# Optimization experiments

Hardware: AMD Instinct MI355X
Metric: run time of the kernel (lower is better)

Reference implementation:

```python
import jax, jax.numpy as jnp
import numpy as np

N_NODES = 20000
N_EDGES = 320000
D_IN = 256
N_CLASS = 10

def _glorot(key, shape):
    fan_in, fan_out = shape[0], shape[1]
    lim = np.sqrt(6.0 / (fan_in + fan_out)).astype(np.float32)
    return jax.random.uniform(key, shape, jnp.float32, -lim, lim)

def setup_inputs() -> dict:
    key = jax.random.key(0)
    ks = jax.random.split(key, 12)
    x = jax.random.normal(ks[0], (N_NODES, D_IN), jnp.float32)
    edge_index = jax.random.randint(ks[1], (2, N_EDGES), 0, N_NODES, jnp.int64)
    return {
        "x": x,
        "edge_index": edge_index,
        # GraphConv 1: num_feature -> 128 (lin_rel on aggregated neighbors, lin_root on self)
        "W1_rel": _glorot(ks[2], (D_IN, 128)),
        "W1_root": _glorot(ks[3], (D_IN, 128)),
        "b1": jnp.zeros((128,), jnp.float32),
        # GraphConv 2: 128 -> 64
        "W2_rel": _glorot(ks[4], (128, 64)),
        "W2_root": _glorot(ks[5], (128, 64)),
        "b2": jnp.zeros((64,), jnp.float32),
        # MLP head
        "lin1_w": _glorot(ks[6], (64, 128)),
        "lin1_b": jnp.zeros((128,), jnp.float32),
        "lin2_w": _glorot(ks[7], (128, 64)),
        "lin2_b": jnp.zeros((64,), jnp.float32),
        "lin3_w": _glorot(ks[8], (64, N_CLASS)),
        "lin3_b": jnp.zeros((N_CLASS,), jnp.float32),
    }

def _graph_conv(x, src, dst, W_rel, W_root, b):
    # PyG GraphConv (aggr='add'): out_i = W_rel @ sum_{j in N(i)} x_j + W_root @ x_i + b
    agg = jax.ops.segment_sum(x[src], dst, num_segments=x.shape[0])  # [N, d_in]
    return agg @ W_rel + x @ W_root + b

def reference(x, edge_index, W1_rel, W1_root, b1, W2_rel, W2_root, b2,
              lin1_w, lin1_b, lin2_w, lin2_b, lin3_w, lin3_b):
    src, dst = edge_index[0], edge_index[1]  # flow: source_to_target
    h = _graph_conv(x, src, dst, W1_rel, W1_root, b1)
    h = jax.nn.relu(h)  # dropout is identity in eval mode
    h = _graph_conv(h, src, dst, W2_rel, W2_root, b2)
    h = jax.nn.relu(h @ lin1_w + lin1_b)
    h = jax.nn.relu(h @ lin2_w + lin2_b)
    return jax.nn.log_softmax(h @ lin3_w + lin3_b, axis=-1)
```

## Files before the change

kernel.cpp:

```cpp
#include <hip/hip_runtime.h>


#define NNODES 20000
#define NEDGES 320000
#define CAP 64

typedef __attribute__((ext_vector_type(8))) short bf16x8;
typedef __attribute__((ext_vector_type(4))) float f32x4;

__device__ inline short f2bf(float f) {
    unsigned u = __builtin_bit_cast(unsigned, f);
    u += 0x7FFFu + ((u >> 16) & 1u);
    return (short)(u >> 16);
}
__device__ inline float bf2f(short h) {
    unsigned u = ((unsigned)(unsigned short)h) << 16;
    return __builtin_bit_cast(float, u);
}

__device__ inline size_t swz_off(int n, int k, int ktiles) {
    return (size_t)((n >> 4) * ktiles + (k >> 5)) * 512 +
           ((((k >> 3) & 3) * 16 + (n & 15)) << 3) + (k & 7);
}

__global__ void prep_kernel(const float* __restrict__ W1r, const float* __restrict__ W1o,
                            const float* __restrict__ W2r, const float* __restrict__ W2o,
                            const float* __restrict__ L1,  const float* __restrict__ L2,
                            short* __restrict__ WT,
                            const float* __restrict__ x, short* __restrict__ XBs,
                            const int* __restrict__ src, const int* __restrict__ dst,
                            int* __restrict__ cnt, int* __restrict__ nbr) {
    const int b = blockIdx.x;
    if (b < 384) {
        int idx = b * 256 + threadIdx.x;
        if (idx < 65536) {
            int n = idx >> 8, k = idx & 255;
            float v = (n < 128) ? W1r[k * 128 + n] : W1o[k * 128 + (n - 128)];
            WT[swz_off(n, k, 8)] = f2bf(v);
        } else if (idx < 65536 + 16384) {
            int i = idx - 65536;
            int n = i >> 7, k = i & 127;
            float v = (n < 64) ? W2r[k * 64 + n] : W2o[k * 64 + (n - 64)];
            WT[65536 + swz_off(n, k, 4)] = f2bf(v);
        } else if (idx < 65536 + 16384 + 8192) {
            int i = idx - (65536 + 16384);
            int n = i >> 6, k = i & 63;
            WT[idx] = f2bf(L1[k * 128 + n]);
        } else {
            int i = idx - (65536 + 16384 + 8192);
            int n = i >> 7, k = i & 127;
            WT[idx] = f2bf(L2[k * 64 + n]);
        }
    } else if (b < 384 + 2500) {
        int t = (b - 384) * 256 + threadIdx.x;
        int row = t >> 5, q = t & 31;
        const float* xp = x + (size_t)row * 256 + q * 8;
        float4 f0 = *reinterpret_cast<const float4*>(xp);
        float4 f1 = *reinterpret_cast<const float4*>(xp + 4);
        bf16x8 o;
        o[0] = f2bf(f0.x); o[1] = f2bf(f0.y); o[2] = f2bf(f0.z); o[3] = f2bf(f0.w);
        o[4] = f2bf(f1.x); o[5] = f2bf(f1.y); o[6] = f2bf(f1.z); o[7] = f2bf(f1.w);
        size_t off = (size_t)((row >> 4) * 8 + (q >> 2)) * 512 +
                     (((q & 3) * 16 + (row & 15)) << 3);
        *reinterpret_cast<bf16x8*>(XBs + off) = o;
    } else {
        int e = (b - 384 - 2500) * 256 + threadIdx.x;
        int d = dst[e];
        int p = atomicAdd(&cnt[d], 1);
        if (p < CAP) nbr[(d << 6) + p] = src[e];
    }
}

__global__ __launch_bounds__(256)
void gemm1_swz(const short* __restrict__ XBs, const short* __restrict__ WT1s,
               const float* __restrict__ b1, short* __restrict__ C1A, int M) {
    const int tid = threadIdx.x;
    const int cb = blockIdx.x & 3;
    const int rb = blockIdx.x >> 2;
    const int wid = tid >> 6, lane = tid & 63;
    const int lr = lane & 15, lg = lane >> 4;
    const int rt = rb * 4 + wid;
    const short* abase = XBs + (size_t)rt * 4096 + lane * 8;
    const short* bbase = WT1s + (size_t)(cb * 4) * 4096 + lane * 8;
    f32x4 acc[4] = {};
    #pragma unroll
    for (int ks = 0; ks < 8; ++ks) {
        bf16x8 a = *reinterpret_cast<const bf16x8*>(abase + ks * 512);
        #pragma unroll
        for (int nt = 0; nt < 4; ++nt) {
            bf16x8 bb = *reinterpret_cast<const bf16x8*>(bbase + (nt * 8 + ks) * 512);
            acc[nt] = __builtin_amdgcn_mfma_f32_16x16x32_bf16(a, bb, acc[nt], 0, 0, 0);
        }
    }
    #pragma unroll
    for (int r = 0; r < 4; ++r) {
        int row = rt * 16 + lg * 4 + r;
        if (row >= M) continue;
        #pragma unroll
        for (int nt = 0; nt < 4; ++nt) {
            int col = cb * 64 + nt * 16 + lr;
            float v = acc[nt][r];
            if (col >= 128) v += b1[col - 128];
            C1A[(size_t)row * 256 + col] = f2bf(v);
        }
    }
}

template<int GPN, int LD, bool RELU, bool SWZ>
__global__ void gather_bf16(const short* __restrict__ base,
                            const int* __restrict__ cnt, const int* __restrict__ nbr,
                            short* __restrict__ outp) {
    const int tid = threadIdx.x;
    const int node = blockIdx.x * (256 / GPN) + tid / GPN;
    const int ci = tid % GPN;
    const int c8 = ci * 8;
    float acc[8];
    bf16x8 iv = *reinterpret_cast<const bf16x8*>(base + (size_t)node * LD + LD / 2 + c8);
    #pragma unroll
    for (int i = 0; i < 8; ++i) acc[i] = bf2f(iv[i]);
    const int beg = node << 6;
    const int deg = min(cnt[node], CAP);
    const int end = beg + deg;
    int j = beg;
    for (; j + 3 < end; j += 4) {
        int s0 = nbr[j], s1 = nbr[j + 1], s2 = nbr[j + 2], s3 = nbr[j + 3];
        bf16x8 v0 = *reinterpret_cast<const bf16x8*>(base + (size_t)s0 * LD + c8);
        bf16x8 v1 = *reinterpret_cast<const bf16x8*>(base + (size_t)s1 * LD + c8);
        bf16x8 v2 = *reinterpret_cast<const bf16x8*>(base + (size_t)s2 * LD + c8);
        bf16x8 v3 = *reinterpret_cast<const bf16x8*>(base + (size_t)s3 * LD + c8);
        #pragma unroll
        for (int i = 0; i < 8; ++i)
            acc[i] += (bf2f(v0[i]) + bf2f(v1[i])) + (bf2f(v2[i]) + bf2f(v3[i]));
    }
    for (; j < end; ++j) {
        int s = nbr[j];
        bf16x8 vv = *reinterpret_cast<const bf16x8*>(base + (size_t)s * LD + c8);
        #pragma unroll
        for (int i = 0; i < 8; ++i) acc[i] += bf2f(vv[i]);
    }
    bf16x8 o;
    #pragma unroll
    for (int i = 0; i < 8; ++i) {
        float vo = RELU ? fmaxf(acc[i], 0.f) : acc[i];
        o[i] = f2bf(vo);
    }
    size_t off;
    if (SWZ) {
        off = (size_t)((node >> 4) * (GPN / 4) + (ci >> 2)) * 512 +
              (((ci & 3) * 16 + (node & 15)) << 3);
    } else {
        off = (size_t)node * (LD / 2) + c8;
    }
    *reinterpret_cast<bf16x8*>(outp + off) = o;
}

__global__ __launch_bounds__(256)
void gemm2_swz(const short* __restrict__ H1s, const short* __restrict__ WT2s,
               const float* __restrict__ b2, short* __restrict__ C2A, int M) {
    const int tid = threadIdx.x;
    const int cb = blockIdx.x & 1;
    const int rb = blockIdx.x >> 1;
    const int wid = tid >> 6, lane = tid & 63;
    const int lr = lane & 15, lg = lane >> 4;
    const int rt = rb * 4 + wid;
    const short* abase = H1s + (size_t)rt * 2048 + lane * 8;
    const short* bbase = WT2s + (size_t)(cb * 4) * 2048 + lane * 8;
    f32x4 acc[4] = {};
    #pragma unroll
    for (int ks = 0; ks < 4; ++ks) {
        bf16x8 a = *reinterpret_cast<const bf16x8*>(abase + ks * 512);
        #pragma unroll
        for (int nt = 0; nt < 4; ++nt) {
            bf16x8 bb = *reinterpret_cast<const bf16x8*>(bbase + (nt * 4 + ks) * 512);
            acc[nt] = __builtin_amdgcn_mfma_f32_16x16x32_bf16(a, bb, acc[nt], 0, 0, 0);
        }
    }
    #pragma unroll
    for (int r = 0; r < 4; ++r) {
        int row = rt * 16 + lg * 4 + r;
        if (row >= M) continue;
        #pragma unroll
        for (int nt = 0; nt < 4; ++nt) {
            int col = cb * 64 + nt * 16 + lr;
            float v = acc[nt][r];
            if (col >= 64) v += b2[col - 64];
            C2A[(size_t)row * 128 + col] = f2bf(v);
        }
    }
}

__global__ __launch_bounds__(256)
void mlp_head(const short* __restrict__ H2,
              const short* __restrict__ WT3, const float* __restrict__ b3,
              const short* __restrict__ WT4, const float* __restrict__ b4,
              const float* __restrict__ W5, const float* __restrict__ b5,
              float* __restrict__ out, int M) {
    __shared__ short H2s[64][72];
    __shared__ short H3s[64][136];
    __shared__ short WU[128 * 72];
    __shared__ short H4s[64][72];
    __shared__ float cb[842];
    const int tid = threadIdx.x;
    const int bm = blockIdx.x * 64;
    const int wid = tid >> 6, lane = tid & 63;
    const int lr = lane & 15, lg = lane >> 4;

    for (int i = tid; i < 842; i += 256) {
        float v;
        if (i < 128) v = b3[i];
        else if (i < 192) v = b4[i - 128];
        else if (i < 832) v = W5[i - 192];
        else v = b5[i - 832];
        cb[i] = v;
    }
    #pragma unroll
    for (int p = 0; p < 4; ++p) {
        int L = tid + p * 256;
        int n = L >> 3;
        int kc = (L & 7) * 8;
        *reinterpret_cast<bf16x8*>(&WU[n * 72 + kc]) =
            *reinterpret_cast<const bf16x8*>(WT3 + (size_t)n * 64 + kc);
    }
    #pragma unroll
    for (int p = 0; p < 2; ++p) {
        int L = tid + p * 256;
        int r = L >> 3;
        int c8 = (L & 7) * 8;
        int node = bm + r;
        bf16x8 v = {};
        if (node < M) v = *reinterpret_cast<const bf16x8*>(H2 + (size_t)node * 64 + c8);
        *reinterpret_cast<bf16x8*>(&H2s[r][c8]) = v;
    }
    __syncthreads();

    {
        f32x4 a1[8] = {};
        #pragma unroll
        for (int ks = 0; ks < 2; ++ks) {
            bf16x8 a = *reinterpret_cast<const bf16x8*>(&H2s[wid * 16 + lr][ks * 32 + lg * 8]);
            #pragma unroll
            for (int nt = 0; nt < 8; ++nt) {
                bf16x8 b = *reinterpret_cast<const bf16x8*>(&WU[(nt * 16 + lr) * 72 + ks * 32 + lg * 8]);
                a1[nt] = __builtin_amdgcn_mfma_f32_16x16x32_bf16(a, b, a1[nt], 0, 0, 0);
            }
        }
        #pragma unroll
        for (int r = 0; r < 4; ++r) {
            int row = wid * 16 + lg * 4 + r;
            #pragma unroll
            for (int nt = 0; nt < 8; ++nt) {
                int col = nt * 16 + lr;
                H3s[row][col] = f2bf(fmaxf(a1[nt][r] + cb[col], 0.f));
            }
        }
    }
    __syncthreads();

    #pragma unroll
    for (int p = 0; p < 4; ++p) {
        int L = tid + p * 256;
        int n = L >> 4;
        int kc = (L & 15) * 8;
        *reinterpret_cast<bf16x8*>(&WU[n * 136 + kc]) =
            *reinterpret_cast<const bf16x8*>(WT4 + (size_t)n * 128 + kc);
    }
    __syncthreads();

    {
        f32x4 a2[4] = {};
        #pragma unroll
        for (int ks = 0; ks < 4; ++ks) {
            bf16x8 a = *reinterpret_cast<const bf16x8*>(&H3s[wid * 16 + lr][ks * 32 + lg * 8]);
            #pragma unroll
            for (int nt = 0; nt < 4; ++nt) {
                bf16x8 b = *reinterpret_cast<const bf16x8*>(&WU[(nt * 16 + lr) * 136 + ks * 32 + lg * 8]);
                a2[nt] = __builtin_amdgcn_mfma_f32_16x16x32_bf16(a, b, a2[nt], 0, 0, 0);
            }
        }
        #pragma unroll
        for (int r = 0; r < 4; ++r) {
            int row = wid * 16 + lg * 4 + r;
            #pragma unroll
            for (int nt = 0; nt < 4; ++nt) {
                int col = nt * 16 + lr;
                H4s[row][col] = f2bf(fmaxf(a2[nt][r] + cb[128 + col], 0.f));
            }
        }
    }
    __syncthreads();

    if (tid < 64) {
        int node = bm + tid;
        if (node < M) {
            float logit[10];
            #pragma unroll
            for (int c = 0; c < 10; ++c) logit[c] = cb[832 + c];
            #pragma unroll
            for (int k = 0; k < 64; ++k) {
                float hv = bf2f(H4s[tid][k]);
                #pragma unroll
                for (int c = 0; c < 10; ++c) logit[c] += hv * cb[192 + k * 10 + c];
            }
            float m = logit[0];
            #pragma unroll
            for (int c = 1; c < 10; ++c) m = fmaxf(m, logit[c]);
            float s = 0.f;
            #pragma unroll
            for (int c = 0; c < 10; ++c) s += expf(logit[c] - m);
            float lse = m + logf(s);
            float* o = out + (size_t)node * 10;
            #pragma unroll
            for (int c = 0; c < 10; ++c) o[c] = logit[c] - lse;
        }
    }
}

extern "C" void kernel_launch(void* const* d_in, const int* in_sizes, int n_in,
                              void* d_out, int out_size, void* d_ws, size_t ws_size,
                              hipStream_t stream) {
    const float* x       = (const float*)d_in[0];
    const int*   edge    = (const int*)d_in[1];
    const int*   src     = edge;
    const int*   dst     = edge + NEDGES;
    const float* W1_rel  = (const float*)d_in[2];
    const float* W1_root = (const float*)d_in[3];
    const float* b1      = (const float*)d_in[4];
    const float* W2_rel  = (const float*)d_in[5];
    const float* W2_root = (const float*)d_in[6];
    const float* b2      = (const float*)d_in[7];
    const float* lin1_w  = (const float*)d_in[8];
    const float* lin1_b  = (const float*)d_in[9];
    const float* lin2_w  = (const float*)d_in[10];
    const float* lin2_b  = (const float*)d_in[11];
    const float* lin3_w  = (const float*)d_in[12];
    const float* lin3_b  = (const float*)d_in[13];
    float* out = (float*)d_out;

    const int M = NNODES;
    char* p = (char*)d_ws;
    auto alloc = [&](size_t bytes) { char* r = p; p += (bytes + 63) & ~63ull; return r; };
    short* WT   = (short*)alloc(98304 * 2);
    short* WT1s = WT;
    short* WT2s = WT1s + 65536;
    short* WT3  = WT2s + 16384;
    short* WT4  = WT3 + 8192;
    short* XBs  = (short*)alloc((size_t)1252 * 4096 * 2);
    short* C1A  = (short*)alloc((size_t)M * 256 * 2);
    short* H1s  = (short*)alloc((size_t)1252 * 2048 * 2);
    short* C2A  = (short*)alloc((size_t)M * 128 * 2);
    short* H2   = (short*)alloc((size_t)M * 64 * 2);
    int* cnt = (int*)alloc(NNODES * 4);
    int* nbr = (int*)alloc((size_t)NNODES * CAP * 4);

    hipMemsetAsync(cnt, 0, NNODES * sizeof(int), stream);
    prep_kernel<<<384 + 2500 + NEDGES / 256, 256, 0, stream>>>(
        W1_rel, W1_root, W2_rel, W2_root, lin1_w, lin2_w, WT, x, XBs,
        src, dst, cnt, nbr);

    gemm1_swz<<<4 * 313, 256, 0, stream>>>(XBs, WT1s, b1, C1A, M);
    gather_bf16<16, 256, true, true><<<NNODES / 16, 256, 0, stream>>>(
        C1A, cnt, nbr, H1s);
    gemm2_swz<<<2 * 313, 256, 0, stream>>>(H1s, WT2s, b2, C2A, M);
    gather_bf16<8, 128, false, false><<<NNODES / 32, 256, 0, stream>>>(
        C2A, cnt, nbr, H2);
    mlp_head<<<(M + 63) / 64, 256, 0, stream>>>(H2, WT3, lin1_b, WT4, lin2_b,
                                                lin3_w, lin3_b, out, M);
}
```

Measured before the change: 94.88 us.

## Fuse neighbor gathers with following GEMM and MLP head kernels

```diff
diff --git a/kernel.cpp b/kernel.cpp
--- a/kernel.cpp
+++ b/kernel.cpp
@@ -106,82 +106,68 @@
     }
 }
 
-template<int GPN, int LD, bool RELU, bool SWZ>
-__global__ void gather_bf16(const short* __restrict__ base,
-                            const int* __restrict__ cnt, const int* __restrict__ nbr,
-                            short* __restrict__ outp) {
+__global__ __launch_bounds__(256)
+void gather1_gemm2(const short* __restrict__ C1A,
+                   const int* __restrict__ cnt, const int* __restrict__ nbr,
+                   const short* __restrict__ WT2s, const float* __restrict__ b2,
+                   short* __restrict__ C2A) {
+    __shared__ short H1s[16][136];
     const int tid = threadIdx.x;
-    const int node = blockIdx.x * (256 / GPN) + tid / GPN;
-    const int ci = tid % GPN;
-    const int c8 = ci * 8;
-    float acc[8];
-    bf16x8 iv = *reinterpret_cast<const bf16x8*>(base + (size_t)node * LD + LD / 2 + c8);
-    #pragma unroll
-    for (int i = 0; i < 8; ++i) acc[i] = bf2f(iv[i]);
-    const int beg = node << 6;
-    const int deg = min(cnt[node], CAP);
-    const int end = beg + deg;
-    int j = beg;
-    for (; j + 3 < end; j += 4) {
-        int s0 = nbr[j], s1 = nbr[j + 1], s2 = nbr[j + 2], s3 = nbr[j + 3];
-        bf16x8 v0 = *reinterpret_cast<const bf16x8*>(base + (size_t)s0 * LD + c8);
-        bf16x8 v1 = *reinterpret_cast<const bf16x8*>(base + (size_t)s1 * LD + c8);
-        bf16x8 v2 = *reinterpret_cast<const bf16x8*>(base + (size_t)s2 * LD + c8);
-        bf16x8 v3 = *reinterpret_cast<const bf16x8*>(base + (size_t)s3 * LD + c8);
-        #pragma unroll
-        for (int i = 0; i < 8; ++i)
-            acc[i] += (bf2f(v0[i]) + bf2f(v1[i])) + (bf2f(v2[i]) + bf2f(v3[i]));
-    }
-    for (; j < end; ++j) {
-        int s = nbr[j];
-        bf16x8 vv = *reinterpret_cast<const bf16x8*>(base + (size_t)s * LD + c8);
-        #pragma unroll
-        for (int i = 0; i < 8; ++i) acc[i] += bf2f(vv[i]);
-    }
-    bf16x8 o;
-    #pragma unroll
-    for (int i = 0; i < 8; ++i) {
-        float vo = RELU ? fmaxf(acc[i], 0.f) : acc[i];
-        o[i] = f2bf(vo);
-    }
-    size_t off;
-    if (SWZ) {
-        off = (size_t)((node >> 4) * (GPN / 4) + (ci >> 2)) * 512 +
-              (((ci & 3) * 16 + (node & 15)) << 3);
-    } else {
-        off = (size_t)node * (LD / 2) + c8;
-    }
-    *reinterpret_cast<bf16x8*>(outp + off) = o;
-}
-
-__global__ __launch_bounds__(256)
-void gemm2_swz(const short* __restrict__ H1s, const short* __restrict__ WT2s,
-               const float* __restrict__ b2, short* __restrict__ C2A, int M) {
-    const int tid = threadIdx.x;
-    const int cb = blockIdx.x & 1;
-    const int rb = blockIdx.x >> 1;
-    const int wid = tid >> 6, lane = tid & 63;
+    const int bm = blockIdx.x * 16;
+
+    {
+        const int node = bm + (tid >> 4);
+        const int c8 = (tid & 15) * 8;
+        float acc[8];
+        bf16x8 iv = *reinterpret_cast<const bf16x8*>(C1A + (size_t)node * 256 + 128 + c8);
+        #pragma unroll
+        for (int i = 0; i < 8; ++i) acc[i] = bf2f(iv[i]);
+        const int beg = node << 6;
+        const int end = beg + min(cnt[node], CAP);
+        int j = beg;
+        for (; j + 3 < end; j += 4) {
+            int s0 = nbr[j], s1 = nbr[j + 1], s2 = nbr[j + 2], s3 = nbr[j + 3];
+            bf16x8 v0 = *reinterpret_cast<const bf16x8*>(C1A + (size_t)s0 * 256 + c8);
+            bf16x8 v1 = *reinterpret_cast<const bf16x8*>(C1A + (size_t)s1 * 256 + c8);
+            bf16x8 v2 = *reinterpret_cast<const bf16x8*>(C1A + (size_t)s2 * 256 + c8);
+            bf16x8 v3 = *reinterpret_cast<const bf16x8*>(C1A + (size_t)s3 * 256 + c8);
+            #pragma unroll
+            for (int i = 0; i < 8; ++i)
+                acc[i] += (bf2f(v0[i]) + bf2f(v1[i])) + (bf2f(v2[i]) + bf2f(v3[i]));
+        }
+        for (; j < end; ++j) {
+            int s = nbr[j];
+            bf16x8 vv = *reinterpret_cast<const bf16x8*>(C1A + (size_t)s * 256 + c8);
+            #pragma unroll
+            for (int i = 0; i < 8; ++i) acc[i] += bf2f(vv[i]);
+        }
+        bf16x8 o;
+        #pragma unroll
+        for (int i = 0; i < 8; ++i) o[i] = f2bf(fmaxf(acc[i], 0.f));
+        *reinterpret_cast<bf16x8*>(&H1s[tid >> 4][c8]) = o;
+    }
+    __syncthreads();
+
+    const int w = tid >> 6, lane = tid & 63;
     const int lr = lane & 15, lg = lane >> 4;
-    const int rt = rb * 4 + wid;
-    const short* abase = H1s + (size_t)rt * 2048 + lane * 8;
-    const short* bbase = WT2s + (size_t)(cb * 4) * 2048 + lane * 8;
-    f32x4 acc[4] = {};
+    f32x4 acc[2] = {};
     #pragma unroll
     for (int ks = 0; ks < 4; ++ks) {
-        bf16x8 a = *reinterpret_cast<const bf16x8*>(abase + ks * 512);
-        #pragma unroll
-        for (int nt = 0; nt < 4; ++nt) {
-            bf16x8 bb = *reinterpret_cast<const bf16x8*>(bbase + (nt * 4 + ks) * 512);
+        bf16x8 a = *reinterpret_cast<const bf16x8*>(&H1s[lr][lg * 8 + ks * 32]);
+        #pragma unroll
+        for (int nt = 0; nt < 2; ++nt) {
+            int ntg = w * 2 + nt;
+            bf16x8 bb = *reinterpret_cast<const bf16x8*>(
+                WT2s + (size_t)(ntg * 4 + ks) * 512 + lane * 8);
             acc[nt] = __builtin_amdgcn_mfma_f32_16x16x32_bf16(a, bb, acc[nt], 0, 0, 0);
         }
     }
     #pragma unroll
     for (int r = 0; r < 4; ++r) {
-        int row = rt * 16 + lg * 4 + r;
-        if (row >= M) continue;
-        #pragma unroll
-        for (int nt = 0; nt < 4; ++nt) {
-            int col = cb * 64 + nt * 16 + lr;
+        int row = bm + lg * 4 + r;
+        #pragma unroll
+        for (int nt = 0; nt < 2; ++nt) {
+            int col = w * 32 + nt * 16 + lr;
             float v = acc[nt][r];
             if (col >= 64) v += b2[col - 64];
             C2A[(size_t)row * 128 + col] = f2bf(v);
@@ -190,19 +176,20 @@
 }
 
 __global__ __launch_bounds__(256)
-void mlp_head(const short* __restrict__ H2,
-              const short* __restrict__ WT3, const float* __restrict__ b3,
-              const short* __restrict__ WT4, const float* __restrict__ b4,
-              const float* __restrict__ W5, const float* __restrict__ b5,
-              float* __restrict__ out, int M) {
-    __shared__ short H2s[64][72];
-    __shared__ short H3s[64][136];
-    __shared__ short WU[128 * 72];
-    __shared__ short H4s[64][72];
+void gather2_mlp(const short* __restrict__ C2A,
+                 const int* __restrict__ cnt, const int* __restrict__ nbr,
+                 const short* __restrict__ WT3, const float* __restrict__ b3,
+                 const short* __restrict__ WT4, const float* __restrict__ b4,
+                 const float* __restrict__ W5, const float* __restrict__ b5,
+                 float* __restrict__ out) {
+    __shared__ short H2s[32][72];
+    __shared__ short H3s[32][136];
+    __shared__ short WU[9216];
+    __shared__ short H4s[32][72];
     __shared__ float cb[842];
     const int tid = threadIdx.x;
-    const int bm = blockIdx.x * 64;
-    const int wid = tid >> 6, lane = tid & 63;
+    const int bm = blockIdx.x * 32;
+    const int w = tid >> 6, lane = tid & 63;
     const int lr = lane & 15, lg = lane >> 4;
 
     for (int i = tid; i < 842; i += 256) {
@@ -221,35 +208,59 @@
         *reinterpret_cast<bf16x8*>(&WU[n * 72 + kc]) =
             *reinterpret_cast<const bf16x8*>(WT3 + (size_t)n * 64 + kc);
     }
-    #pragma unroll
-    for (int p = 0; p < 2; ++p) {
-        int L = tid + p * 256;
-        int r = L >> 3;
-        int c8 = (L & 7) * 8;
-        int node = bm + r;
-        bf16x8 v = {};
-        if (node < M) v = *reinterpret_cast<const bf16x8*>(H2 + (size_t)node * 64 + c8);
-        *reinterpret_cast<bf16x8*>(&H2s[r][c8]) = v;
-    }
-    __syncthreads();
 
     {
-        f32x4 a1[8] = {};
+        const int node = bm + (tid >> 3);
+        const int c8 = (tid & 7) * 8;
+        float acc[8];
+        bf16x8 iv = *reinterpret_cast<const bf16x8*>(C2A + (size_t)node * 128 + 64 + c8);
+        #pragma unroll
+        for (int i = 0; i < 8; ++i) acc[i] = bf2f(iv[i]);
+        const int beg = node << 6;
+        const int end = beg + min(cnt[node], CAP);
+        int j = beg;
+        for (; j + 3 < end; j += 4) {
+            int s0 = nbr[j], s1 = nbr[j + 1], s2 = nbr[j + 2], s3 = nbr[j + 3];
+            bf16x8 v0 = *reinterpret_cast<const bf16x8*>(C2A + (size_t)s0 * 128 + c8);
+            bf16x8 v1 = *reinterpret_cast<const bf16x8*>(C2A + (size_t)s1 * 128 + c8);
+            bf16x8 v2 = *reinterpret_cast<const bf16x8*>(C2A + (size_t)s2 * 128 + c8);
+            bf16x8 v3 = *reinterpret_cast<const bf16x8*>(C2A + (size_t)s3 * 128 + c8);
+            #pragma unroll
+            for (int i = 0; i < 8; ++i)
+                acc[i] += (bf2f(v0[i]) + bf2f(v1[i])) + (bf2f(v2[i]) + bf2f(v3[i]));
+        }
+        for (; j < end; ++j) {
+            int s = nbr[j];
+            bf16x8 vv = *reinterpret_cast<const bf16x8*>(C2A + (size_t)s * 128 + c8);
+            #pragma unroll
+            for (int i = 0; i < 8; ++i) acc[i] += bf2f(vv[i]);
+        }
+        bf16x8 o;
+        #pragma unroll
+        for (int i = 0; i < 8; ++i) o[i] = f2bf(acc[i]);
+        *reinterpret_cast<bf16x8*>(&H2s[tid >> 3][c8]) = o;
+    }
+    __syncthreads();
+
+    {
+        const int rb = (w >> 1) * 16, cbse = (w & 1) * 64;
+        f32x4 a1[4] = {};
         #pragma unroll
         for (int ks = 0; ks < 2; ++ks) {
-            bf16x8 a = *reinterpret_cast<const bf16x8*>(&H2s[wid * 16 + lr][ks * 32 + lg * 8]);
-            #pragma unroll
-            for (int nt = 0; nt < 8; ++nt) {
-                bf16x8 b = *reinterpret_cast<const bf16x8*>(&WU[(nt * 16 + lr) * 72 + ks * 32 + lg * 8]);
+            bf16x8 a = *reinterpret_cast<const bf16x8*>(&H2s[rb + lr][ks * 32 + lg * 8]);
+            #pragma unroll
+            for (int nt = 0; nt < 4; ++nt) {
+                bf16x8 b = *reinterpret_cast<const bf16x8*>(
+                    &WU[(cbse + nt * 16 + lr) * 72 + ks * 32 + lg * 8]);
                 a1[nt] = __builtin_amdgcn_mfma_f32_16x16x32_bf16(a, b, a1[nt], 0, 0, 0);
             }
         }
         #pragma unroll
         for (int r = 0; r < 4; ++r) {
-            int row = wid * 16 + lg * 4 + r;
-            #pragma unroll
-            for (int nt = 0; nt < 8; ++nt) {
-                int col = nt * 16 + lr;
+            int row = rb + lg * 4 + r;
+            #pragma unroll
+            for (int nt = 0; nt < 4; ++nt) {
+                int col = cbse + nt * 16 + lr;
                 H3s[row][col] = f2bf(fmaxf(a1[nt][r] + cb[col], 0.f));
             }
         }
@@ -267,51 +278,51 @@
     __syncthreads();
 
     {
-        f32x4 a2[4] = {};
+        const int rb = (w >> 1) * 16, cbse = (w & 1) * 32;
+        f32x4 a2[2] = {};
         #pragma unroll
         for (int ks = 0; ks < 4; ++ks) {
-            bf16x8 a = *reinterpret_cast<const bf16x8*>(&H3s[wid * 16 + lr][ks * 32 + lg * 8]);
-            #pragma unroll
-            for (int nt = 0; nt < 4; ++nt) {
-                bf16x8 b = *reinterpret_cast<const bf16x8*>(&WU[(nt * 16 + lr) * 136 + ks * 32 + lg * 8]);
+            bf16x8 a = *reinterpret_cast<const bf16x8*>(&H3s[rb + lr][ks * 32 + lg * 8]);
+            #pragma unroll
+            for (int nt = 0; nt < 2; ++nt) {
+                bf16x8 b = *reinterpret_cast<const bf16x8*>(
+                    &WU[(cbse + nt * 16 + lr) * 136 + ks * 32 + lg * 8]);
                 a2[nt] = __builtin_amdgcn_mfma_f32_16x16x32_bf16(a, b, a2[nt], 0, 0, 0);
             }
         }
         #pragma unroll
         for (int r = 0; r < 4; ++r) {
-            int row = wid * 16 + lg * 4 + r;
-            #pragma unroll
-            for (int nt = 0; nt < 4; ++nt) {
-                int col = nt * 16 + lr;
+            int row = rb + lg * 4 + r;
+            #pragma unroll
+            for (int nt = 0; nt < 2; ++nt) {
+                int col = cbse + nt * 16 + lr;
                 H4s[row][col] = f2bf(fmaxf(a2[nt][r] + cb[128 + col], 0.f));
             }
         }
     }
     __syncthreads();
 
-    if (tid < 64) {
+    if (tid < 32) {
         int node = bm + tid;
-        if (node < M) {
-            float logit[10];
-            #pragma unroll
-            for (int c = 0; c < 10; ++c) logit[c] = cb[832 + c];
-            #pragma unroll
-            for (int k = 0; k < 64; ++k) {
-                float hv = bf2f(H4s[tid][k]);
-                #pragma unroll
-                for (int c = 0; c < 10; ++c) logit[c] += hv * cb[192 + k * 10 + c];
-            }
-            float m = logit[0];
-            #pragma unroll
-            for (int c = 1; c < 10; ++c) m = fmaxf(m, logit[c]);
-            float s = 0.f;
-            #pragma unroll
-            for (int c = 0; c < 10; ++c) s += expf(logit[c] - m);
-            float lse = m + logf(s);
-            float* o = out + (size_t)node * 10;
-            #pragma unroll
-            for (int c = 0; c < 10; ++c) o[c] = logit[c] - lse;
-        }
+        float logit[10];
+        #pragma unroll
+        for (int c = 0; c < 10; ++c) logit[c] = cb[832 + c];
+        #pragma unroll
+        for (int k = 0; k < 64; ++k) {
+            float hv = bf2f(H4s[tid][k]);
+            #pragma unroll
+            for (int c = 0; c < 10; ++c) logit[c] += hv * cb[192 + k * 10 + c];
+        }
+        float m = logit[0];
+        #pragma unroll
+        for (int c = 1; c < 10; ++c) m = fmaxf(m, logit[c]);
+        float s = 0.f;
+        #pragma unroll
+        for (int c = 0; c < 10; ++c) s += expf(logit[c] - m);
+        float lse = m + logf(s);
+        float* o = out + (size_t)node * 10;
+        #pragma unroll
+        for (int c = 0; c < 10; ++c) o[c] = logit[c] - lse;
     }
 }
 
@@ -346,9 +357,7 @@
     short* WT4  = WT3 + 8192;
     short* XBs  = (short*)alloc((size_t)1252 * 4096 * 2);
     short* C1A  = (short*)alloc((size_t)M * 256 * 2);
-    short* H1s  = (short*)alloc((size_t)1252 * 2048 * 2);
     short* C2A  = (short*)alloc((size_t)M * 128 * 2);
-    short* H2   = (short*)alloc((size_t)M * 64 * 2);
     int* cnt = (int*)alloc(NNODES * 4);
     int* nbr = (int*)alloc((size_t)NNODES * CAP * 4);
 
@@ -358,11 +367,7 @@
         src, dst, cnt, nbr);
 
     gemm1_swz<<<4 * 313, 256, 0, stream>>>(XBs, WT1s, b1, C1A, M);
-    gather_bf16<16, 256, true, true><<<NNODES / 16, 256, 0, stream>>>(
-        C1A, cnt, nbr, H1s);
-    gemm2_swz<<<2 * 313, 256, 0, stream>>>(H1s, WT2s, b2, C2A, M);
-    gather_bf16<8, 128, false, false><<<NNODES / 32, 256, 0, stream>>>(
-        C2A, cnt, nbr, H2);
-    mlp_head<<<(M + 63) / 64, 256, 0, stream>>>(H2, WT3, lin1_b, WT4, lin2_b,
-                                                lin3_w, lin3_b, out, M);
-}
+    gather1_gemm2<<<NNODES / 16, 256, 0, stream>>>(C1A, cnt, nbr, WT2s, b2, C2A);
+    gather2_mlp<<<NNODES / 32, 256, 0, stream>>>(C2A, cnt, nbr, WT3, lin1_b,
+                                                 WT4, lin2_b, lin3_w, lin3_b, out);
+}
```

After: 79.71 us, median of 2. 1.19x faster.
